# Performance work log

Measured on AMD Instinct MI355X. Metric: run time of the kernel, lower is better.

The kernel has to match this reference:

```python
import jax, jax.numpy as jnp
import numpy as np
import math

B, N, F_IN, F_OUT = 8, 2048, 128, 128


def _uniform(key, shape, stdv):
    return jax.random.uniform(key, shape, dtype=jnp.float32, minval=-stdv, maxval=stdv)


def setup_inputs() -> dict:
    key = jax.random.key(0)
    k_x, k_a, k_w, k_att, k_bw, k_ba = jax.random.split(key, 6)
    X = jax.random.normal(k_x, (B, N, F_IN), dtype=jnp.float32)
    # dense 0/1 adjacency, as consumed by torch.bmm(A, ...)
    A = jax.random.randint(k_a, (B, N, N), 0, 2).astype(jnp.float32)
    stdv_W = 1.0 / math.sqrt(F_OUT)        # W.size(1) == n_fea_out
    stdv_a = 1.0 / math.sqrt(2 * F_OUT)    # a.size(1) == 2*n_fea_out
    W = _uniform(k_w, (F_IN, F_OUT), stdv_W)
    a = _uniform(k_att, (1, 2 * F_OUT), stdv_a)
    bias_W = _uniform(k_bw, (F_OUT,), stdv_W)
    bias_a = _uniform(k_ba, (N,), stdv_a)
    return {"X": X, "A": A, "W": W, "a": a, "bias_a": bias_a, "bias_W": bias_W}


def reference(X, A, W, a, bias_a, bias_W):
    # XW: [B, N, F_out]
    XW = jnp.einsum('bnf,fo->bno', X, W)
    f = W.shape[1]
    # Original materializes Z[b,i,j] = concat(XW[b,j], XW[b,i]) then dots with a.
    # This is separable: Z1[b,i,j] = a[:f]@XW[b,j] + a[f:]@XW[b,i] + bias_a[j]
    a_j = a[0, :f]   # multiplies XW[b, j]
    a_i = a[0, f:]   # multiplies XW[b, i]
    s_j = jnp.einsum('bnf,f->bn', XW, a_j)  # [B, N]
    s_i = jnp.einsum('bnf,f->bn', XW, a_i)  # [B, N]
    Z1 = s_i[:, :, None] + s_j[:, None, :] + bias_a[None, None, :]  # [B, N, N]
    den = jnp.exp(Z1)
    num = jnp.einsum('bik,bkj->bij', A, den)  # torch.bmm(A, denominator)
    # where numerator == 0 the torch code leaves att uninitialized; use 0 deterministically
    nz = num != 0
    att = jnp.where(nz, den / jnp.where(nz, num, 1.0), 0.0)
    buf = jnp.einsum('bij,bjf->bif', att, XW)
    H = jnp.einsum('bij,bjf->bif', A, buf) + bias_W
    return H
```

## Files before the change

kernel.cpp:

```cpp
#include <hip/hip_runtime.h>

#define BB 8
#define NN 2048
#define FF 128


__global__ __launch_bounds__(256) void k1_p_xsum(const float* __restrict__ X,
                                                 const float* __restrict__ W,
                                                 const float* __restrict__ a,
                                                 float* __restrict__ p,
                                                 float* __restrict__ xpart) {
    __shared__ float wls[FF];
    __shared__ float xls[FF];
    int t = threadIdx.x;
    if (t < FF) {
        float s = 0.f;
#pragma unroll 8
        for (int f = 0; f < FF; ++f) s += W[t * FF + f] * a[FF + f];
        wls[t] = s;
        xls[t] = 0.f;
    }
    __syncthreads();

    int gr0 = blockIdx.x * 32;
    int lane = t & 63;
    int wave = t >> 6;
    int half = lane >> 5;
    int l32 = lane & 31;

    float4 wv = ((const float4*)wls)[l32];
    float4 cs = make_float4(0.f, 0.f, 0.f, 0.f);
    const float4* X4 = (const float4*)(X + (size_t)gr0 * FF);

#pragma unroll
    for (int it = 0; it < 4; ++it) {
        int rloc = wave * 8 + it * 2 + half;
        float4 xv = X4[(size_t)rloc * 32 + l32];
        cs.x += xv.x; cs.y += xv.y; cs.z += xv.z; cs.w += xv.w;
        float s = xv.x * wv.x + xv.y * wv.y + xv.z * wv.z + xv.w * wv.w;
#pragma unroll
        for (int off = 16; off; off >>= 1) s += __shfl_xor(s, off, 64);
        if (l32 == 0) p[(size_t)gr0 + rloc] = expf(s);
    }

    atomicAdd(&xls[l32 * 4 + 0], cs.x);
    atomicAdd(&xls[l32 * 4 + 1], cs.y);
    atomicAdd(&xls[l32 * 4 + 2], cs.z);
    atomicAdd(&xls[l32 * 4 + 3], cs.w);
    __syncthreads();
    if (t < FF) xpart[blockIdx.x * FF + t] = xls[t];
}

__global__ __launch_bounds__(256) void k3_r(const float* __restrict__ A,
                                            const float* __restrict__ W,
                                            const float* __restrict__ xpart,
                                            const float* __restrict__ p,
                                            float* __restrict__ r,
                                            float* __restrict__ S,
                                            unsigned long long* __restrict__ pk) {
    __shared__ float p_lds[NN];
    int t = threadIdx.x;

    if (blockIdx.x == 0) {
#pragma unroll
        for (int k = 0; k < 4; ++k) {
            int o = t + 256 * k;
            int b = o >> 7, f = o & 127;
            float s = 0.f;
            for (int j = 0; j < 64; ++j) s += xpart[(b * 64 + j) * FF + f];
            p_lds[o] = s;
        }
        __syncthreads();
#pragma unroll
        for (int k = 0; k < 4; ++k) {
            int o = t + 256 * k;
            int b = o >> 7, f = o & 127;
            float s = 0.f;
#pragma unroll 8
            for (int c = 0; c < FF; ++c) s += p_lds[b * FF + c] * W[c * FF + f];
            S[o] = s;
        }
        return;
    }

    int row0 = (blockIdx.x - 1) * 8;
    int b = row0 >> 11;

    const float4* p4 = (const float4*)(p + (size_t)b * NN);
    float4* pl4 = (float4*)p_lds;
    pl4[t]       = p4[t];
    pl4[t + 256] = p4[t + 256];
    __syncthreads();

    int lane = t & 63;
    int wave = t >> 6;
    int rowA = row0 + wave * 2;
    int rowB = rowA + 1;
    const float4* Aa = (const float4*)(A + (size_t)rowA * NN);
    const float4* Ab = (const float4*)(A + (size_t)rowB * NN);

    int c = lane & 3;
    float accA = 0.f, accB = 0.f;
#pragma unroll
    for (int it = 0; it < 8; ++it) {
        float4 pv = pl4[it * 64 + lane];
        float4 va = Aa[it * 64 + lane];
        float4 vb = Ab[it * 64 + lane];
        accA += va.x * pv.x + va.y * pv.y + va.z * pv.z + va.w * pv.w;
        accB += vb.x * pv.x + vb.y * pv.y + vb.z * pv.z + vb.w * pv.w;

        unsigned long long a0 = __ballot(va.x != 0.f);
        unsigned long long a1 = __ballot(va.y != 0.f);
        unsigned long long a2 = __ballot(va.z != 0.f);
        unsigned long long a3 = __ballot(va.w != 0.f);
        unsigned long long b0 = __ballot(vb.x != 0.f);
        unsigned long long b1 = __ballot(vb.y != 0.f);
        unsigned long long b2 = __ballot(vb.z != 0.f);
        unsigned long long b3 = __ballot(vb.w != 0.f);
        if (lane < 8) {
            unsigned long long alo = (c & 1) ? a1 : a0;
            unsigned long long ahi = (c & 1) ? a3 : a2;
            unsigned long long am  = (c & 2) ? ahi : alo;
            unsigned long long blo = (c & 1) ? b1 : b0;
            unsigned long long bhi = (c & 1) ? b3 : b2;
            unsigned long long bm  = (c & 2) ? bhi : blo;
            int row = (lane < 4) ? rowA : rowB;
            unsigned long long m = (lane < 4) ? am : bm;
            pk[(size_t)row * 32 + it * 4 + c] = m;
        }
    }
#pragma unroll
    for (int off = 32; off; off >>= 1) {
        accA += __shfl_xor(accA, off, 64);
        accB += __shfl_xor(accB, off, 64);
    }

    if (lane == 0) {
        r[rowA] = (accA != 0.f) ? (p_lds[rowA & (NN - 1)] / accA) : 0.f;
        r[rowB] = (accB != 0.f) ? (p_lds[rowB & (NN - 1)] / accB) : 0.f;
    }
}

__global__ __launch_bounds__(256) void k4_H(const unsigned long long* __restrict__ pk,
                                            const float* __restrict__ rr,
                                            const float* __restrict__ S,
                                            const float* __restrict__ bias_W,
                                            float* __restrict__ Hout) {
    __shared__ float r_lds[NN];
    __shared__ float s_lds[FF];
    __shared__ float bw_lds[FF];
    int row0 = blockIdx.x * 8;
    int b = row0 >> 11;

    const float4* r4 = (const float4*)(rr + (size_t)b * NN);
    float4* rl4 = (float4*)r_lds;
    rl4[threadIdx.x]       = r4[threadIdx.x];
    rl4[threadIdx.x + 256] = r4[threadIdx.x + 256];
    if (threadIdx.x < FF) {
        s_lds[threadIdx.x]  = S[b * FF + threadIdx.x];
        bw_lds[threadIdx.x] = bias_W[threadIdx.x];
    }
    __syncthreads();

    int lane = threadIdx.x & 63;
    int wave = threadIdx.x >> 6;
    int rowA = row0 + wave * 2;
    int rowB = rowA + 1;

    unsigned long long w =
        pk[(size_t)(lane < 32 ? rowA : rowB) * 32 + (lane & 31)];

    float accA = 0.f, accB = 0.f;
#pragma unroll
    for (int it = 0; it < 8; ++it) {
        float4 rv = rl4[it * 64 + lane];
        unsigned long long mA0 = __shfl(w, it * 4 + 0, 64);
        unsigned long long mA1 = __shfl(w, it * 4 + 1, 64);
        unsigned long long mA2 = __shfl(w, it * 4 + 2, 64);
        unsigned long long mA3 = __shfl(w, it * 4 + 3, 64);
        unsigned long long mB0 = __shfl(w, 32 + it * 4 + 0, 64);
        unsigned long long mB1 = __shfl(w, 32 + it * 4 + 1, 64);
        unsigned long long mB2 = __shfl(w, 32 + it * 4 + 2, 64);
        unsigned long long mB3 = __shfl(w, 32 + it * 4 + 3, 64);
        if ((mA0 >> lane) & 1ull) accA += rv.x;
        if ((mA1 >> lane) & 1ull) accA += rv.y;
        if ((mA2 >> lane) & 1ull) accA += rv.z;
        if ((mA3 >> lane) & 1ull) accA += rv.w;
        if ((mB0 >> lane) & 1ull) accB += rv.x;
        if ((mB1 >> lane) & 1ull) accB += rv.y;
        if ((mB2 >> lane) & 1ull) accB += rv.z;
        if ((mB3 >> lane) & 1ull) accB += rv.w;
    }
#pragma unroll
    for (int off = 32; off; off >>= 1) {
        accA += __shfl_xor(accA, off, 64);
        accB += __shfl_xor(accB, off, 64);
    }

    float2 sv = ((const float2*)s_lds)[lane];
    float2 bv = ((const float2*)bw_lds)[lane];
    float2* H2 = (float2*)Hout;
    float2 ha, hb;
    ha.x = accA * sv.x + bv.x;  ha.y = accA * sv.y + bv.y;
    hb.x = accB * sv.x + bv.x;  hb.y = accB * sv.y + bv.y;
    H2[(size_t)rowA * 64 + lane] = ha;
    H2[(size_t)rowB * 64 + lane] = hb;
}

extern "C" void kernel_launch(void* const* d_in, const int* in_sizes, int n_in,
                              void* d_out, int out_size, void* d_ws, size_t ws_size,
                              hipStream_t stream) {
    const float* X      = (const float*)d_in[0];
    const float* A      = (const float*)d_in[1];
    const float* W      = (const float*)d_in[2];
    const float* a      = (const float*)d_in[3];
    const float* bias_W = (const float*)d_in[5];
    float* out = (float*)d_out;

    float* ws    = (float*)d_ws;
    float* xpart = ws;
    float* S     = ws + 65536;
    float* p     = ws + 66560;
    float* r     = ws + 82944;
    unsigned long long* pk = (unsigned long long*)(ws + 99328);

    k1_p_xsum<<<(BB * NN) / 32, 256, 0, stream>>>(X, W, a, p, xpart);
    k3_r<<<(BB * NN) / 8 + 1, 256, 0, stream>>>(A, W, xpart, p, r, S, pk);
    k4_H<<<(BB * NN) / 8, 256, 0, stream>>>(pk, r, S, bias_W, out);
}
```

Before: 236.2 us.

## Pack adjacency bitmask per lane and issue all A row loads upfront

The packed adjacency mask changes from wave-wide 64-bit ballots to a per-lane 32-bit word holding each lane's own 4×8 nonzero bits. This removes the ballots and selects in k3 and the cross-lane shuffles in k4. k3 now issues all sixteen float4 loads of A before computing, behind a scheduling barrier, to keep more memory requests in flight at the cost of registers. The W·a precompute in k1 is also vectorised with float4 loads. The mask footprint is unchanged, but its layout is now lane-major.

Result: faster. 227.5 us, median of 2 (-3.7%).

```diff
diff --git a/kernel.cpp b/kernel.cpp
--- a/kernel.cpp
+++ b/kernel.cpp
@@ -7,40 +7,42 @@
 
 __global__ __launch_bounds__(256) void k1_p_xsum(const float* __restrict__ X,
                                                  const float* __restrict__ W,
-                                                 const float* __restrict__ a,
+                                                 const float* __restrict__ av,
                                                  float* __restrict__ p,
                                                  float* __restrict__ xpart) {
     __shared__ float wls[FF];
     __shared__ float xls[FF];
-    int t = threadIdx.x;
+    const int t = threadIdx.x;
     if (t < FF) {
+        const float4* W4 = (const float4*)(W + t * FF);
+        const float4* a4 = (const float4*)(av + FF);
         float s = 0.f;
-#pragma unroll 8
-        for (int f = 0; f < FF; ++f) s += W[t * FF + f] * a[FF + f];
+#pragma unroll
+        for (int f = 0; f < FF / 4; ++f) {
+            const float4 w4 = W4[f], aa = a4[f];
+            s += w4.x * aa.x + w4.y * aa.y + w4.z * aa.z + w4.w * aa.w;
+        }
         wls[t] = s;
         xls[t] = 0.f;
     }
     __syncthreads();
 
-    int gr0 = blockIdx.x * 32;
-    int lane = t & 63;
-    int wave = t >> 6;
-    int half = lane >> 5;
-    int l32 = lane & 31;
-
-    float4 wv = ((const float4*)wls)[l32];
+    const int gr0 = blockIdx.x * 32;
+    const int lane = t & 63, wave = t >> 6;
+    const int half = lane >> 5, l32 = lane & 31;
+    const float4 wv = ((const float4*)wls)[l32];
     float4 cs = make_float4(0.f, 0.f, 0.f, 0.f);
     const float4* X4 = (const float4*)(X + (size_t)gr0 * FF);
 
 #pragma unroll
     for (int it = 0; it < 4; ++it) {
-        int rloc = wave * 8 + it * 2 + half;
-        float4 xv = X4[(size_t)rloc * 32 + l32];
+        const int rloc = wave * 8 + it * 2 + half;
+        const float4 xv = X4[(size_t)rloc * 32 + l32];
         cs.x += xv.x; cs.y += xv.y; cs.z += xv.z; cs.w += xv.w;
         float s = xv.x * wv.x + xv.y * wv.y + xv.z * wv.z + xv.w * wv.w;
 #pragma unroll
         for (int off = 16; off; off >>= 1) s += __shfl_xor(s, off, 64);
-        if (l32 == 0) p[(size_t)gr0 + rloc] = expf(s);
+        if (l32 == 0) p[gr0 + rloc] = expf(s);
     }
 
     atomicAdd(&xls[l32 * 4 + 0], cs.x);
@@ -57,15 +59,15 @@
                                             const float* __restrict__ p,
                                             float* __restrict__ r,
                                             float* __restrict__ S,
-                                            unsigned long long* __restrict__ pk) {
+                                            unsigned* __restrict__ pk) {
     __shared__ float p_lds[NN];
-    int t = threadIdx.x;
+    const int t = threadIdx.x;
 
     if (blockIdx.x == 0) {
 #pragma unroll
         for (int k = 0; k < 4; ++k) {
-            int o = t + 256 * k;
-            int b = o >> 7, f = o & 127;
+            const int o = t + 256 * k;
+            const int b = o >> 7, f = o & 127;
             float s = 0.f;
             for (int j = 0; j < 64; ++j) s += xpart[(b * 64 + j) * FF + f];
             p_lds[o] = s;
@@ -73,8 +75,8 @@
         __syncthreads();
 #pragma unroll
         for (int k = 0; k < 4; ++k) {
-            int o = t + 256 * k;
-            int b = o >> 7, f = o & 127;
+            const int o = t + 256 * k;
+            const int b = o >> 7, f = o & 127;
             float s = 0.f;
 #pragma unroll 8
             for (int c = 0; c < FF; ++c) s += p_lds[b * FF + c] * W[c * FF + f];
@@ -83,113 +85,94 @@
         return;
     }
 
-    int row0 = (blockIdx.x - 1) * 8;
-    int b = row0 >> 11;
-
+    const int row0 = (blockIdx.x - 1) * 8;
+    const int b = row0 >> 11;
     const float4* p4 = (const float4*)(p + (size_t)b * NN);
     float4* pl4 = (float4*)p_lds;
     pl4[t]       = p4[t];
     pl4[t + 256] = p4[t + 256];
     __syncthreads();
 
-    int lane = t & 63;
-    int wave = t >> 6;
-    int rowA = row0 + wave * 2;
-    int rowB = rowA + 1;
+    const int lane = t & 63, wave = t >> 6;
+    const int rowA = row0 + wave * 2;
+    const int rowB = rowA + 1;
     const float4* Aa = (const float4*)(A + (size_t)rowA * NN);
     const float4* Ab = (const float4*)(A + (size_t)rowB * NN);
 
-    int c = lane & 3;
+    const float4 va0 = Aa[0 * 64 + lane], va1 = Aa[1 * 64 + lane];
+    const float4 va2 = Aa[2 * 64 + lane], va3 = Aa[3 * 64 + lane];
+    const float4 va4 = Aa[4 * 64 + lane], va5 = Aa[5 * 64 + lane];
+    const float4 va6 = Aa[6 * 64 + lane], va7 = Aa[7 * 64 + lane];
+    const float4 vb0 = Ab[0 * 64 + lane], vb1 = Ab[1 * 64 + lane];
+    const float4 vb2 = Ab[2 * 64 + lane], vb3 = Ab[3 * 64 + lane];
+    const float4 vb4 = Ab[4 * 64 + lane], vb5 = Ab[5 * 64 + lane];
+    const float4 vb6 = Ab[6 * 64 + lane], vb7 = Ab[7 * 64 + lane];
+    __builtin_amdgcn_sched_barrier(0);
+
     float accA = 0.f, accB = 0.f;
-#pragma unroll
-    for (int it = 0; it < 8; ++it) {
-        float4 pv = pl4[it * 64 + lane];
-        float4 va = Aa[it * 64 + lane];
-        float4 vb = Ab[it * 64 + lane];
-        accA += va.x * pv.x + va.y * pv.y + va.z * pv.z + va.w * pv.w;
-        accB += vb.x * pv.x + vb.y * pv.y + vb.z * pv.z + vb.w * pv.w;
-
-        unsigned long long a0 = __ballot(va.x != 0.f);
-        unsigned long long a1 = __ballot(va.y != 0.f);
-        unsigned long long a2 = __ballot(va.z != 0.f);
-        unsigned long long a3 = __ballot(va.w != 0.f);
-        unsigned long long b0 = __ballot(vb.x != 0.f);
-        unsigned long long b1 = __ballot(vb.y != 0.f);
-        unsigned long long b2 = __ballot(vb.z != 0.f);
-        unsigned long long b3 = __ballot(vb.w != 0.f);
-        if (lane < 8) {
-            unsigned long long alo = (c & 1) ? a1 : a0;
-            unsigned long long ahi = (c & 1) ? a3 : a2;
-            unsigned long long am  = (c & 2) ? ahi : alo;
-            unsigned long long blo = (c & 1) ? b1 : b0;
-            unsigned long long bhi = (c & 1) ? b3 : b2;
-            unsigned long long bm  = (c & 2) ? bhi : blo;
-            int row = (lane < 4) ? rowA : rowB;
-            unsigned long long m = (lane < 4) ? am : bm;
-            pk[(size_t)row * 32 + it * 4 + c] = m;
-        }
-    }
+    unsigned mA = 0u, mB = 0u;
+#define STEP(K, VA, VB) {                                                     \
+        const float4 pv = pl4[K * 64 + lane];                                 \
+        accA += VA.x * pv.x + VA.y * pv.y + VA.z * pv.z + VA.w * pv.w;        \
+        accB += VB.x * pv.x + VB.y * pv.y + VB.z * pv.z + VB.w * pv.w;        \
+        const unsigned na = (VA.x != 0.f ? 1u : 0u) | (VA.y != 0.f ? 2u : 0u) \
+                          | (VA.z != 0.f ? 4u : 0u) | (VA.w != 0.f ? 8u : 0u);\
+        const unsigned nb = (VB.x != 0.f ? 1u : 0u) | (VB.y != 0.f ? 2u : 0u) \
+                          | (VB.z != 0.f ? 4u : 0u) | (VB.w != 0.f ? 8u : 0u);\
+        mA |= na << (K * 4); mB |= nb << (K * 4); }
+    STEP(0, va0, vb0) STEP(1, va1, vb1) STEP(2, va2, vb2) STEP(3, va3, vb3)
+    STEP(4, va4, vb4) STEP(5, va5, vb5) STEP(6, va6, vb6) STEP(7, va7, vb7)
+#undef STEP
+
+    pk[(size_t)rowA * 64 + lane] = mA;
+    pk[(size_t)rowB * 64 + lane] = mB;
+
 #pragma unroll
     for (int off = 32; off; off >>= 1) {
         accA += __shfl_xor(accA, off, 64);
         accB += __shfl_xor(accB, off, 64);
     }
-
     if (lane == 0) {
-        r[rowA] = (accA != 0.f) ? (p_lds[rowA & (NN - 1)] / accA) : 0.f;
-        r[rowB] = (accB != 0.f) ? (p_lds[rowB & (NN - 1)] / accB) : 0.f;
-    }
-}
-
-__global__ __launch_bounds__(256) void k4_H(const unsigned long long* __restrict__ pk,
+        const int lr = rowA & (NN - 1);
+        r[rowA] = (accA != 0.f) ? (p_lds[lr] / accA) : 0.f;
+        r[rowB] = (accB != 0.f) ? (p_lds[lr + 1] / accB) : 0.f;
+    }
+}
+
+__global__ __launch_bounds__(256) void k4_H(const unsigned* __restrict__ pk,
                                             const float* __restrict__ rr,
                                             const float* __restrict__ S,
                                             const float* __restrict__ bias_W,
                                             float* __restrict__ Hout) {
     __shared__ float r_lds[NN];
-    __shared__ float s_lds[FF];
-    __shared__ float bw_lds[FF];
-    int row0 = blockIdx.x * 8;
-    int b = row0 >> 11;
+    __shared__ float sls[FF], bwls[FF];
+    const int t = threadIdx.x;
+    const int row0 = blockIdx.x * 8;
+    const int b = row0 >> 11;
 
     const float4* r4 = (const float4*)(rr + (size_t)b * NN);
     float4* rl4 = (float4*)r_lds;
-    rl4[threadIdx.x]       = r4[threadIdx.x];
-    rl4[threadIdx.x + 256] = r4[threadIdx.x + 256];
-    if (threadIdx.x < FF) {
-        s_lds[threadIdx.x]  = S[b * FF + threadIdx.x];
-        bw_lds[threadIdx.x] = bias_W[threadIdx.x];
-    }
-    __syncthreads();
-
-    int lane = threadIdx.x & 63;
-    int wave = threadIdx.x >> 6;
-    int rowA = row0 + wave * 2;
-    int rowB = rowA + 1;
-
-    unsigned long long w =
-        pk[(size_t)(lane < 32 ? rowA : rowB) * 32 + (lane & 31)];
+    rl4[t]       = r4[t];
+    rl4[t + 256] = r4[t + 256];
+    if (t < FF) { sls[t] = S[b * FF + t]; bwls[t] = bias_W[t]; }
+    __syncthreads();
+
+    const int lane = t & 63, wave = t >> 6;
+    const int rowA = row0 + wave * 2;
+    const int rowB = rowA + 1;
+    const unsigned wA = pk[(size_t)rowA * 64 + lane];
+    const unsigned wB = pk[(size_t)rowB * 64 + lane];
 
     float accA = 0.f, accB = 0.f;
 #pragma unroll
     for (int it = 0; it < 8; ++it) {
-        float4 rv = rl4[it * 64 + lane];
-        unsigned long long mA0 = __shfl(w, it * 4 + 0, 64);
-        unsigned long long mA1 = __shfl(w, it * 4 + 1, 64);
-        unsigned long long mA2 = __shfl(w, it * 4 + 2, 64);
-        unsigned long long mA3 = __shfl(w, it * 4 + 3, 64);
-        unsigned long long mB0 = __shfl(w, 32 + it * 4 + 0, 64);
-        unsigned long long mB1 = __shfl(w, 32 + it * 4 + 1, 64);
-        unsigned long long mB2 = __shfl(w, 32 + it * 4 + 2, 64);
-        unsigned long long mB3 = __shfl(w, 32 + it * 4 + 3, 64);
-        if ((mA0 >> lane) & 1ull) accA += rv.x;
-        if ((mA1 >> lane) & 1ull) accA += rv.y;
-        if ((mA2 >> lane) & 1ull) accA += rv.z;
-        if ((mA3 >> lane) & 1ull) accA += rv.w;
-        if ((mB0 >> lane) & 1ull) accB += rv.x;
-        if ((mB1 >> lane) & 1ull) accB += rv.y;
-        if ((mB2 >> lane) & 1ull) accB += rv.z;
-        if ((mB3 >> lane) & 1ull) accB += rv.w;
+        const float4 rv = rl4[it * 64 + lane];
+        const unsigned na = (wA >> (it * 4)) & 15u;
+        const unsigned nb = (wB >> (it * 4)) & 15u;
+        accA += (na & 1u) ? rv.x : 0.f;  accB += (nb & 1u) ? rv.x : 0.f;
+        accA += (na & 2u) ? rv.y : 0.f;  accB += (nb & 2u) ? rv.y : 0.f;
+        accA += (na & 4u) ? rv.z : 0.f;  accB += (nb & 4u) ? rv.z : 0.f;
+        accA += (na & 8u) ? rv.w : 0.f;  accB += (nb & 8u) ? rv.w : 0.f;
     }
 #pragma unroll
     for (int off = 32; off; off >>= 1) {
@@ -197,14 +180,11 @@
         accB += __shfl_xor(accB, off, 64);
     }
 
-    float2 sv = ((const float2*)s_lds)[lane];
-    float2 bv = ((const float2*)bw_lds)[lane];
+    const float2 sv = ((const float2*)sls)[lane];
+    const float2 bv = ((const float2*)bwls)[lane];
     float2* H2 = (float2*)Hout;
-    float2 ha, hb;
-    ha.x = accA * sv.x + bv.x;  ha.y = accA * sv.y + bv.y;
-    hb.x = accB * sv.x + bv.x;  hb.y = accB * sv.y + bv.y;
-    H2[(size_t)rowA * 64 + lane] = ha;
-    H2[(size_t)rowB * 64 + lane] = hb;
+    H2[(size_t)rowA * 64 + lane] = make_float2(accA * sv.x + bv.x, accA * sv.y + bv.y);
+    H2[(size_t)rowB * 64 + lane] = make_float2(accB * sv.x + bv.x, accB * sv.y + bv.y);
 }
 
 extern "C" void kernel_launch(void* const* d_in, const int* in_sizes, int n_in,
@@ -222,7 +202,7 @@
     float* S     = ws + 65536;
     float* p     = ws + 66560;
     float* r     = ws + 82944;
-    unsigned long long* pk = (unsigned long long*)(ws + 99328);
+    unsigned* pk = (unsigned*)(ws + 99328);
 
     k1_p_xsum<<<(BB * NN) / 32, 256, 0, stream>>>(X, W, a, p, xpart);
     k3_r<<<(BB * NN) / 8 + 1, 256, 0, stream>>>(A, W, xpart, p, r, S, pk);
```
